# Performance work log

Hardware: AMD Instinct MI355X
Metric: run time of the kernel (lower is better)

## Reference

```python
import jax, jax.numpy as jnp
import numpy as np

WAY, NQ, C, FS = 5, 4096, 64, 5
T = FS * FS            # 25 spatial tokens
EMB = T + 1            # feature_size**2 + feature_proj_dim = 26
HEADS = 2
HD = EMB // HEADS      # 13
SCALE = HD ** -0.5
T_ATTN = 5.0           # args.temperature_attn
TEMP = 0.2             # args.temperature
LN_EPS = 1e-6


def _ln(x, g, b):
    m = x.mean(-1, keepdims=True)
    v = jnp.mean((x - m) ** 2, axis=-1, keepdims=True)
    return (x - m) / jnp.sqrt(v + LN_EPS) * g + b


def _block(x, p):
    # pre-LN transformer block (timm-style), x: (B, T, EMB)
    h = _ln(x, p['ln1_g'], p['ln1_b'])
    qkv = h @ p['qkv_w'].T + p['qkv_b']                       # (B,T,3*EMB)
    B, N, _ = qkv.shape
    qkv = qkv.reshape(B, N, 3, HEADS, HD).transpose(2, 0, 3, 1, 4)
    q, k, v = qkv[0], qkv[1], qkv[2]                          # (B,H,T,hd)
    a = jax.nn.softmax(jnp.einsum('bhqd,bhkd->bhqk', q, k) * SCALE, axis=-1)
    o = jnp.einsum('bhqk,bhkd->bhqd', a, v).transpose(0, 2, 1, 3).reshape(B, N, EMB)
    x = x + o @ p['attn_w'].T + p['attn_b']
    h = _ln(x, p['ln2_g'], p['ln2_b'])
    h = jax.nn.gelu(h @ p['fc1_w'].T + p['fc1_b'], approximate=False)
    return x + h @ p['fc2_w'].T + p['fc2_b']


def _decoder(corr, src, tgt, p):
    # CATs TransformerAggregator, num_hyperpixel=1, depth=1
    # corr: (B,1,T,T); src/tgt: (B,1,T,1) projected features
    pos = jnp.concatenate([
        jnp.broadcast_to(p['pos_x'], (1, 1, FS, FS, EMB // 2)),
        jnp.broadcast_to(p['pos_y'], (1, 1, FS, FS, EMB // 2))], axis=-1).reshape(1, 1, T, EMB)
    B = corr.shape[0]
    x = jnp.concatenate([jnp.swapaxes(corr, -1, -2), tgt], axis=3) + pos
    x = _block(x.reshape(B, T, EMB), p)
    x = (x @ p['dec_w'].T + p['dec_b']).reshape(B, 1, T, T)
    x = jnp.swapaxes(x, -1, -2) + corr            # swap axes for second self-attn pass
    x = jnp.concatenate([x, src], axis=3) + pos
    x = _block(x.reshape(B, T, EMB), p)           # same block weights reused
    x = (x @ p['dec_w'].T + p['dec_b']).reshape(B, 1, T, T) + corr
    return x.mean(axis=1)                         # (B,T,T)


def _forward(spt, qry, proj_w, proj_b, pos_x, pos_y, ln1_g, ln1_b, qkv_w, qkv_b,
             attn_w, attn_b, ln2_g, ln2_b, fc1_w, fc1_b, fc2_w, fc2_b, dec_w, dec_b):
    p = dict(pos_x=pos_x, pos_y=pos_y, ln1_g=ln1_g, ln1_b=ln1_b, qkv_w=qkv_w,
             qkv_b=qkv_b, attn_w=attn_w, attn_b=attn_b, ln2_g=ln2_g, ln2_b=ln2_b,
             fc1_w=fc1_w, fc1_b=fc1_b, fc2_w=fc2_w, fc2_b=fc2_b, dec_w=dec_w, dec_b=dec_b)
    # normalize_feature: subtract channel mean
    spt = spt - spt.mean(axis=1, keepdims=True)
    qry = qry - qry.mean(axis=1, keepdims=True)
    spt_f = jnp.broadcast_to(spt[None], (NQ, WAY, C, FS, FS)).reshape(-1, C, FS, FS)
    qry_f = jnp.broadcast_to(qry[:, None], (NQ, WAY, C, FS, FS)).reshape(-1, C, FS, FS)

    def l2n(x):  # FeatureL2Norm over channel dim
        return x / jnp.sqrt(jnp.sum(x * x, axis=1, keepdims=True) + 1e-6)

    s = l2n(spt_f).reshape(-1, C, T)
    t = l2n(qry_f).reshape(-1, C, T)
    corr = jnp.einsum('bci,bcj->bij', s, t)[:, None]                  # (B,1,T,T)
    sp = (jnp.swapaxes(spt_f.reshape(-1, C, T), 1, 2) @ proj_w.T + proj_b)[:, None]
    tp = (jnp.swapaxes(qry_f.reshape(-1, C, T), 1, 2) @ proj_w.T + proj_b)[:, None]
    refined = _decoder(corr, sp, tp, p)                               # (B,T,T)

    corr_s = refined.reshape(NQ, WAY, T, FS, FS)
    corr_q = refined.reshape(NQ, WAY, FS, FS, T)

    def gnorm(x, axis):  # torch.var is unbiased (ddof=1)
        m = x.mean(axis=axis, keepdims=True)
        v = jnp.var(x, axis=axis, keepdims=True, ddof=1)
        return (x - m) / jnp.sqrt(v + 1e-5)

    corr_s = jax.nn.softmax(gnorm(corr_s, 2) / T_ATTN, axis=2).reshape(NQ, WAY, FS, FS, FS, FS)
    corr_q = jax.nn.softmax(gnorm(corr_q, 4) / T_ATTN, axis=4).reshape(NQ, WAY, FS, FS, FS, FS)
    attn_s = corr_s.sum(axis=(4, 5))                                  # (NQ,WAY,FS,FS)
    attn_q = corr_q.sum(axis=(2, 3))
    spt_att = attn_s[:, :, None] * spt[None]                          # (NQ,WAY,C,FS,FS)
    qry_att = attn_q[:, :, None] * qry[:, None]
    sp_p = spt_att.mean(axis=(-1, -2))                                # (NQ,WAY,C)
    qp_p = qry_att.mean(axis=(-1, -2))
    n1 = jnp.maximum(jnp.linalg.norm(sp_p, axis=-1), 1e-8)
    n2 = jnp.maximum(jnp.linalg.norm(qp_p, axis=-1), 1e-8)
    sim = jnp.sum(sp_p * qp_p, axis=-1) / (n1 * n2)                   # (NQ,WAY)
    return sim / TEMP


def setup_inputs() -> dict:
    key = jax.random.key(0)
    ks = jax.random.split(key, 12)

    def w(i, shape, s=0.02):
        return jax.random.normal(ks[i], shape, jnp.float32) * s

    return {
        'spt': jax.random.normal(ks[0], (WAY, C, FS, FS), jnp.float32),
        'qry': jax.random.normal(ks[1], (NQ, C, FS, FS), jnp.float32),
        'proj_w': w(2, (1, C)), 'proj_b': jnp.zeros((1,), jnp.float32),
        'pos_x': w(3, (1, 1, 1, FS, EMB // 2)),
        'pos_y': w(4, (1, 1, FS, 1, EMB // 2)),
        'ln1_g': jnp.ones((EMB,), jnp.float32), 'ln1_b': jnp.zeros((EMB,), jnp.float32),
        'qkv_w': w(5, (3 * EMB, EMB)), 'qkv_b': jnp.zeros((3 * EMB,), jnp.float32),
        'attn_w': w(6, (EMB, EMB)), 'attn_b': jnp.zeros((EMB,), jnp.float32),
        'ln2_g': jnp.ones((EMB,), jnp.float32), 'ln2_b': jnp.zeros((EMB,), jnp.float32),
        'fc1_w': w(7, (4 * EMB, EMB)), 'fc1_b': jnp.zeros((4 * EMB,), jnp.float32),
        'fc2_w': w(8, (EMB, 4 * EMB)), 'fc2_b': jnp.zeros((EMB,), jnp.float32),
        'dec_w': w(9, (T, EMB)), 'dec_b': jnp.zeros((T,), jnp.float32),
    }


def reference(spt, qry, proj_w, proj_b, pos_x, pos_y, ln1_g, ln1_b, qkv_w, qkv_b,
              attn_w, attn_b, ln2_g, ln2_b, fc1_w, fc1_b, fc2_w, fc2_b, dec_w, dec_b):
    return _forward(spt, qry, proj_w, proj_b, pos_x, pos_y, ln1_g, ln1_b, qkv_w, qkv_b,
                    attn_w, attn_b, ln2_g, ln2_b, fc1_w, fc1_b, fc2_w, fc2_b, dec_w, dec_b)
```

## Files before the change

### kernel.cpp

```cpp
#include <hip/hip_runtime.h>
#include <math.h>

#define WAYS 5
#define NQN 4096
#define NBATCH (NQN*WAYS)
#define SAB 68

#define WS_SC 0
#define WS_RS 8000
#define WS_SP 8125
#define WS_QM 8250
#define WS_QR 110650
#define WS_TP 213050

#define P_L1G 0
#define P_L1B 26
#define P_L2G 52
#define P_L2B 78
#define P_QKVB 104
#define P_ATTB 182
#define P_FC1B 208
#define P_FC2B 312
#define P_DECB 338
#define P_TOT 363

__global__ void prep_spt(const float* __restrict__ spt, const float* __restrict__ proj_w,
                         const float* __restrict__ proj_b, float* __restrict__ ws) {
    int tid = threadIdx.x;
    if (tid >= 125) return;
    int w = tid / 25, i = tid % 25;
    const float* base = spt + w * 1600 + i;
    float s = 0.f;
    for (int c = 0; c < 64; c++) s += base[c * 25];
    float m = s * (1.f / 64.f);
    float ss = 0.f, pj = 0.f;
    for (int c = 0; c < 64; c++) {
        float v = base[c * 25] - m;
        ss += v * v; pj += v * proj_w[c];
        ws[WS_SC + (w * 25 + i) * 64 + c] = v;
    }
    ws[WS_RS + w * 25 + i] = rsqrtf(ss + 1e-6f);
    ws[WS_SP + w * 25 + i] = pj + proj_b[0];
}

__global__ void prep_qry(const float* __restrict__ qry, const float* __restrict__ proj_w,
                         const float* __restrict__ proj_b, float* __restrict__ ws) {
    int idx = blockIdx.x * 256 + threadIdx.x;
    if (idx >= NQN * 25) return;
    int q = idx / 25, j = idx % 25;
    const float* base = qry + q * 1600 + j;
    float s = 0.f;
    for (int c = 0; c < 64; c++) s += base[c * 25];
    float m = s * (1.f / 64.f);
    float ss = 0.f, pj = 0.f;
    for (int c = 0; c < 64; c++) {
        float v = base[c * 25] - m;
        ss += v * v; pj += v * proj_w[c];
    }
    ws[WS_QM + idx] = m;
    ws[WS_QR + idx] = rsqrtf(ss + 1e-6f);
    ws[WS_TP + idx] = pj + proj_b[0];
}

template<int M, int N, int K, int TM, int TN, int SA, int WN, int WK, int SO, int VW,
         bool ADD, bool GELU>
__device__ __forceinline__ void mm(const float* __restrict__ A, const float* __restrict__ W,
                                   const float* __restrict__ bias, float* __restrict__ O,
                                   float scale, int tid) {
    static_assert(M % TM == 0 && N % TN == 0, "tile");
    static_assert(VW == 1 || (WK == 1 && K % VW == 0 && SA % VW == 0 && WN % VW == 0), "vec");
    constexpr int GM = M / TM, GN = N / TN;
    for (int v = tid; v < GM * GN; v += 256) {
        const int m0 = (v / GN) * TM, n0 = (v % GN) * TN;
        float acc[TM][TN];
#pragma unroll
        for (int a = 0; a < TM; a++)
#pragma unroll
            for (int c = 0; c < TN; c++) acc[a][c] = 0.f;

        if constexpr (VW == 4) {
#pragma unroll
            for (int k = 0; k < K; k += 4) {
                float4 av[TM], wv[TN];
#pragma unroll
                for (int a = 0; a < TM; a++) av[a] = *(const float4*)(A + (m0 + a) * SA + k);
#pragma unroll
                for (int c = 0; c < TN; c++) wv[c] = *(const float4*)(W + (n0 + c) * WN + k);
#pragma unroll
                for (int a = 0; a < TM; a++)
#pragma unroll
                    for (int c = 0; c < TN; c++) {
                        acc[a][c] += av[a].x * wv[c].x;
                        acc[a][c] += av[a].y * wv[c].y;
                        acc[a][c] += av[a].z * wv[c].z;
                        acc[a][c] += av[a].w * wv[c].w;
                    }
            }
        } else if constexpr (VW == 2) {
#pragma unroll 4
            for (int k = 0; k < K; k += 2) {
                float2 av[TM], wv[TN];
#pragma unroll
                for (int a = 0; a < TM; a++) av[a] = *(const float2*)(A + (m0 + a) * SA + k);
#pragma unroll
                for (int c = 0; c < TN; c++) wv[c] = *(const float2*)(W + (n0 + c) * WN + k);
#pragma unroll
                for (int a = 0; a < TM; a++)
#pragma unroll
                    for (int c = 0; c < TN; c++) {
                        acc[a][c] += av[a].x * wv[c].x;
                        acc[a][c] += av[a].y * wv[c].y;
                    }
            }
        } else {
#pragma unroll 4
            for (int k = 0; k < K; k++) {
                float av[TM], wv[TN];
#pragma unroll
                for (int a = 0; a < TM; a++) av[a] = A[(m0 + a) * SA + k];
#pragma unroll
                for (int c = 0; c < TN; c++) wv[c] = W[(n0 + c) * WN + k * WK];
#pragma unroll
                for (int a = 0; a < TM; a++)
#pragma unroll
                    for (int c = 0; c < TN; c++) acc[a][c] += av[a] * wv[c];
            }
        }
#pragma unroll
        for (int a = 0; a < TM; a++)
#pragma unroll
            for (int c = 0; c < TN; c++) {
                int n = n0 + c;
                float r = acc[a][c] * scale + (bias ? bias[n] : 0.f);
                if (GELU) r = 0.5f * r * (1.f + erff(r * 0.70710678118654752f));
                if (ADD) O[(m0 + a) * SO + n] += r; else O[(m0 + a) * SO + n] = r;
            }
    }
}

__device__ __forceinline__ void ln_row(const float* __restrict__ x, float* __restrict__ h,
                                       const float* __restrict__ g, const float* __restrict__ bb) {
    float s = 0.f;
#pragma unroll
    for (int e = 0; e < 26; e++) s += x[e];
    float m = s * (1.f / 26.f);
    float vv = 0.f;
#pragma unroll
    for (int e = 0; e < 26; e++) { float d = x[e] - m; vv += d * d; }
    float r = rsqrtf(vv * (1.f / 26.f) + 1e-6f);
#pragma unroll
    for (int e = 0; e < 26; e++) h[e] = (x[e] - m) * r * g[e] + bb[e];
}

__device__ __forceinline__ void xblock(float* __restrict__ xm, float* __restrict__ hm,
                                       float* __restrict__ scr, float* __restrict__ ym,
                                       const float* __restrict__ cpar,
                                       const float* __restrict__ qkv_w,
                                       const float* __restrict__ attn_w,
                                       const float* __restrict__ fc1_w,
                                       const float* __restrict__ fc2_w, int tid) {
    if (tid < 25) ln_row(xm + tid * 26, hm + tid * 26, cpar + P_L1G, cpar + P_L1B);
    __syncthreads();
    mm<25, 78, 26, 5, 3, 26, 26, 1, 78, 2, false, false>(hm, qkv_w, cpar + P_QKVB, scr, 1.f, tid);
    __syncthreads();
    {
        const float SC = 0.27735009811261457f;
        for (int v = tid; v < 250; v += 256) {
            int h = v / 125, r = v % 125;
            int m0 = (r / 25) * 5, j = r % 25;
            const float* kb = scr + j * 78 + 26 + h * 13;
            float acc[5] = {0.f, 0.f, 0.f, 0.f, 0.f};
#pragma unroll
            for (int k = 0; k < 13; k++) {
                float kv = kb[k];
#pragma unroll
                for (int a = 0; a < 5; a++) acc[a] += scr[(m0 + a) * 78 + h * 13 + k] * kv;
            }
            float* orow = ym + h * 625;
#pragma unroll
            for (int a = 0; a < 5; a++) orow[(m0 + a) * 25 + j] = acc[a] * SC;
        }
    }
    __syncthreads();
    if (tid < 50) {
        float* row = ym + (tid / 25) * 625 + (tid % 25) * 25;
        float mx = row[0];
        for (int j = 1; j < 25; j++) mx = fmaxf(mx, row[j]);
        float s = 0.f;
        for (int j = 0; j < 25; j++) { float e = __expf(row[j] - mx); row[j] = e; s += e; }
        float inv = 1.f / s;
        for (int j = 0; j < 25; j++) row[j] *= inv;
    }
    __syncthreads();
    for (int v = tid; v < 130; v += 256) {
        int h = v / 65, r = v % 65;
        int m0 = (r / 13) * 5, n = r % 13;
        const float* P = ym + h * 625;
        float acc[5] = {0.f, 0.f, 0.f, 0.f, 0.f};
#pragma unroll
        for (int k = 0; k < 25; k++) {
            float vv = scr[k * 78 + 52 + h * 13 + n];
#pragma unroll
            for (int a = 0; a < 5; a++) acc[a] += P[(m0 + a) * 25 + k] * vv;
        }
#pragma unroll
        for (int a = 0; a < 5; a++) scr[1950 + (m0 + a) * 26 + h * 13 + n] = acc[a];
    }
    __syncthreads();
    mm<25, 26, 26, 5, 2, 26, 26, 1, 26, 2, true, false>(scr + 1950, attn_w, cpar + P_ATTB, xm, 1.f, tid);
    __syncthreads();
    if (tid < 25) ln_row(xm + tid * 26, hm + tid * 26, cpar + P_L2G, cpar + P_L2B);
    __syncthreads();
    mm<25, 104, 26, 5, 4, 26, 26, 1, 104, 2, false, true>(hm, fc1_w, cpar + P_FC1B, scr, 1.f, tid);
    __syncthreads();
    mm<25, 26, 104, 5, 2, 104, 104, 1, 26, 2, true, false>(scr, fc2_w, cpar + P_FC2B, xm, 1.f, tid);
    __syncthreads();
}

__global__ void __launch_bounds__(256, 4)
fused_kernel(const float* __restrict__ qry, const float* __restrict__ ws,
             const float* __restrict__ pos_x, const float* __restrict__ pos_y,
             const float* __restrict__ qkv_w, const float* __restrict__ qkv_b,
             const float* __restrict__ attn_w, const float* __restrict__ attn_b,
             const float* __restrict__ ln1_g, const float* __restrict__ ln1_b,
             const float* __restrict__ ln2_g, const float* __restrict__ ln2_b,
             const float* __restrict__ fc1_w, const float* __restrict__ fc1_b,
             const float* __restrict__ fc2_w, const float* __restrict__ fc2_b,
             const float* __restrict__ dec_w, const float* __restrict__ dec_b,
             float* __restrict__ out) {
    __shared__ __align__(16) float sc[25 * SAB];
    __shared__ __align__(16) float tcb[25 * SAB];
    __shared__ float rsv[25], rtv[25], spv[25], tpv[25];
    __shared__ __align__(16) float corrm[625];
    __shared__ __align__(16) float xm[650];
    __shared__ __align__(16) float hm[650];
    __shared__ __align__(16) float scr[2600];
    __shared__ __align__(16) float ym[1250];
    __shared__ float asv[25], aqv[25];
    __shared__ __align__(16) float cpar[P_TOT];

    const int b = blockIdx.x, q = b / WAYS, w = b % WAYS, tid = threadIdx.x;

    if (tid < 26) {
        cpar[P_L1G + tid] = ln1_g[tid]; cpar[P_L1B + tid] = ln1_b[tid];
        cpar[P_L2G + tid] = ln2_g[tid]; cpar[P_L2B + tid] = ln2_b[tid];
        cpar[P_ATTB + tid] = attn_b[tid]; cpar[P_FC2B + tid] = fc2_b[tid];
    }
    if (tid < 78) cpar[P_QKVB + tid] = qkv_b[tid];
    if (tid < 104) cpar[P_FC1B + tid] = fc1_b[tid];
    if (tid < 25) cpar[P_DECB + tid] = dec_b[tid];

    for (int e = tid; e < 1600; e += 256) {
        int i = e >> 6, c = e & 63;
        sc[i * SAB + c] = ws[WS_SC + w * 1600 + e] * ws[WS_RS + w * 25 + i];
    }
    if (tid < 25) {
        rsv[tid] = ws[WS_RS + w * 25 + tid];
        spv[tid] = ws[WS_SP + w * 25 + tid];
        rtv[tid] = ws[WS_QR + q * 25 + tid];
        tpv[tid] = ws[WS_TP + q * 25 + tid];
    }
    for (int e = tid; e < 1600; e += 256) {
        int c = e / 25, j = e % 25;
        tcb[j * SAB + c] = (qry[q * 1600 + e] - ws[WS_QM + q * 25 + j]) * ws[WS_QR + q * 25 + j];
    }
    __syncthreads();

    mm<25, 25, 64, 5, 1, SAB, SAB, 1, 25, 4, false, false>(sc, tcb, nullptr, corrm, 1.f, tid);
    __syncthreads();

    for (int e = tid; e < 650; e += 256) {
        int t = e / 26, d = e % 26;
        float p = (d < 13) ? pos_x[(t % 5) * 13 + d] : pos_y[(t / 5) * 13 + (d - 13)];
        float base = (d < 25) ? corrm[d * 25 + t] : tpv[t];
        xm[e] = base + p;
    }
    __syncthreads();

    xblock(xm, hm, scr, ym, cpar, qkv_w, attn_w, fc1_w, fc2_w, tid);

    mm<25, 25, 26, 5, 1, 26, 26, 1, 25, 2, false, false>(xm, dec_w, cpar + P_DECB, ym, 1.f, tid);
    __syncthreads();

    for (int e = tid; e < 650; e += 256) {
        int t = e / 26, d = e % 26;
        float p = (d < 13) ? pos_x[(t % 5) * 13 + d] : pos_y[(t / 5) * 13 + (d - 13)];
        float base = (d < 25) ? (ym[d * 25 + t] + corrm[t * 25 + d]) : spv[t];
        xm[e] = base + p;
    }
    __syncthreads();

    xblock(xm, hm, scr, ym, cpar, qkv_w, attn_w, fc1_w, fc2_w, tid);

    mm<25, 25, 26, 5, 1, 26, 26, 1, 25, 2, false, false>(xm, dec_w, cpar + P_DECB, ym, 1.f, tid);
    __syncthreads();
    for (int e = tid; e < 625; e += 256) ym[e] += corrm[e];
    __syncthreads();

    if (tid < 25) {
        int j = tid;
        float s = 0.f;
        for (int i = 0; i < 25; i++) s += ym[i * 25 + j];
        float m = s * 0.04f;
        float ss = 0.f;
        for (int i = 0; i < 25; i++) { float d = ym[i * 25 + j] - m; ss += d * d; }
        float rinv = rsqrtf(ss * (1.f / 24.f) + 1e-5f) * 0.2f;
        float mx = -1e30f;
        for (int i = 0; i < 25; i++) { float z = (ym[i * 25 + j] - m) * rinv; corrm[i * 25 + j] = z; mx = fmaxf(mx, z); }
        float se = 0.f;
        for (int i = 0; i < 25; i++) { float e2 = __expf(corrm[i * 25 + j] - mx); corrm[i * 25 + j] = e2; se += e2; }
        float inv = 1.f / se;
        for (int i = 0; i < 25; i++) corrm[i * 25 + j] *= inv;
    }
    __syncthreads();
    if (tid < 25) {
        int i = tid; float s = 0.f;
        for (int j = 0; j < 25; j++) s += corrm[i * 25 + j];
        asv[i] = s * 0.04f / rsv[i];
    }
    __syncthreads();
    if (tid < 25) {
        int i = tid;
        float s = 0.f;
        for (int j = 0; j < 25; j++) s += ym[i * 25 + j];
        float m = s * 0.04f;
        float ss = 0.f;
        for (int j = 0; j < 25; j++) { float d = ym[i * 25 + j] - m; ss += d * d; }
        float rinv = rsqrtf(ss * (1.f / 24.f) + 1e-5f) * 0.2f;
        float mx = -1e30f;
        for (int j = 0; j < 25; j++) { float z = (ym[i * 25 + j] - m) * rinv; corrm[i * 25 + j] = z; mx = fmaxf(mx, z); }
        float se = 0.f;
        for (int j = 0; j < 25; j++) { float e2 = __expf(corrm[i * 25 + j] - mx); corrm[i * 25 + j] = e2; se += e2; }
        float inv = 1.f / se;
        for (int j = 0; j < 25; j++) corrm[i * 25 + j] *= inv;
    }
    __syncthreads();
    if (tid < 25) {
        int j = tid; float s = 0.f;
        for (int i = 0; i < 25; i++) s += corrm[i * 25 + j];
        aqv[j] = s * 0.04f / rtv[j];
    }
    __syncthreads();

    if (tid < 64) {
        float s = 0.f;
        for (int i = 0; i < 25; i++) s += asv[i] * sc[i * SAB + tid];
        ym[tid] = s;
        float s2 = 0.f;
        for (int j = 0; j < 25; j++) s2 += aqv[j] * tcb[j * SAB + tid];
        ym[64 + tid] = s2;
    }
    __syncthreads();
    if (tid == 0) {
        float d = 0.f, n1 = 0.f, n2 = 0.f;
        for (int c = 0; c < 64; c++) {
            float a = ym[c], bb2 = ym[64 + c];
            d += a * bb2; n1 += a * a; n2 += bb2 * bb2;
        }
        n1 = fmaxf(sqrtf(n1), 1e-8f);
        n2 = fmaxf(sqrtf(n2), 1e-8f);
        out[b] = d / (n1 * n2) * 5.f;
    }
}

extern "C" void kernel_launch(void* const* d_in, const int* in_sizes, int n_in,
                              void* d_out, int out_size, void* d_ws, size_t ws_size,
                              hipStream_t stream) {
    const float* spt    = (const float*)d_in[0];
    const float* qry    = (const float*)d_in[1];
    const float* proj_w = (const float*)d_in[2];
    const float* proj_b = (const float*)d_in[3];
    const float* pos_x  = (const float*)d_in[4];
    const float* pos_y  = (const float*)d_in[5];
    const float* ln1_g  = (const float*)d_in[6];
    const float* ln1_b  = (const float*)d_in[7];
    const float* qkv_w  = (const float*)d_in[8];
    const float* qkv_b  = (const float*)d_in[9];
    const float* attn_w = (const float*)d_in[10];
    const float* attn_b = (const float*)d_in[11];
    const float* ln2_g  = (const float*)d_in[12];
    const float* ln2_b  = (const float*)d_in[13];
    const float* fc1_w  = (const float*)d_in[14];
    const float* fc1_b  = (const float*)d_in[15];
    const float* fc2_w  = (const float*)d_in[16];
    const float* fc2_b  = (const float*)d_in[17];
    const float* dec_w  = (const float*)d_in[18];
    const float* dec_b  = (const float*)d_in[19];
    float* ws  = (float*)d_ws;
    float* out = (float*)d_out;

    prep_spt<<<1, 128, 0, stream>>>(spt, proj_w, proj_b, ws);
    prep_qry<<<(NQN * 25 + 255) / 256, 256, 0, stream>>>(qry, proj_w, proj_b, ws);
    fused_kernel<<<NBATCH, 256, 0, stream>>>(qry, ws, pos_x, pos_y, qkv_w, qkv_b, attn_w, attn_b,
                                             ln1_g, ln1_b, ln2_g, ln2_b, fc1_w, fc1_b,
                                             fc2_w, fc2_b, dec_w, dec_b, out);
}
```

Before: 1.279 ms.

## Shrink shared memory footprint to raise occupancy and split MLP into halves

Removes the staged parameter cache and the hm buffer and reuses ym and scr regions for the LN output and the attention output. The MLP hidden layer is split into two 52-wide chunks so the scratch buffer can shrink, and launch bounds are raised to 5 blocks per CU. The final cosine reduction now uses a wavefront shuffle instead of a serial single-thread loop. The MLP split adds an extra barrier pair per block, and bias and LN parameters are now read from global memory rather than LDS.

```diff
diff --git a/kernel.cpp b/kernel.cpp
--- a/kernel.cpp
+++ b/kernel.cpp
@@ -12,17 +12,6 @@
 #define WS_QM 8250
 #define WS_QR 110650
 #define WS_TP 213050
-
-#define P_L1G 0
-#define P_L1B 26
-#define P_L2G 52
-#define P_L2B 78
-#define P_QKVB 104
-#define P_ATTB 182
-#define P_FC1B 208
-#define P_FC2B 312
-#define P_DECB 338
-#define P_TOT 363
 
 __global__ void prep_spt(const float* __restrict__ spt, const float* __restrict__ proj_w,
                          const float* __restrict__ proj_b, float* __restrict__ ws) {
@@ -152,16 +141,17 @@
     for (int e = 0; e < 26; e++) h[e] = (x[e] - m) * r * g[e] + bb[e];
 }
 
-__device__ __forceinline__ void xblock(float* __restrict__ xm, float* __restrict__ hm,
-                                       float* __restrict__ scr, float* __restrict__ ym,
-                                       const float* __restrict__ cpar,
-                                       const float* __restrict__ qkv_w,
-                                       const float* __restrict__ attn_w,
-                                       const float* __restrict__ fc1_w,
-                                       const float* __restrict__ fc2_w, int tid) {
-    if (tid < 25) ln_row(xm + tid * 26, hm + tid * 26, cpar + P_L1G, cpar + P_L1B);
-    __syncthreads();
-    mm<25, 78, 26, 5, 3, 26, 26, 1, 78, 2, false, false>(hm, qkv_w, cpar + P_QKVB, scr, 1.f, tid);
+__device__ __forceinline__ void xblock(
+        float* __restrict__ xm, float* __restrict__ scr, float* __restrict__ ym,
+        const float* __restrict__ qkv_w, const float* __restrict__ qkv_b,
+        const float* __restrict__ attn_w, const float* __restrict__ attn_b,
+        const float* __restrict__ ln1_g, const float* __restrict__ ln1_b,
+        const float* __restrict__ ln2_g, const float* __restrict__ ln2_b,
+        const float* __restrict__ fc1_w, const float* __restrict__ fc1_b,
+        const float* __restrict__ fc2_w, const float* __restrict__ fc2_b, int tid) {
+    if (tid < 25) ln_row(xm + tid * 26, ym + tid * 26, ln1_g, ln1_b);
+    __syncthreads();
+    mm<25, 78, 26, 5, 3, 26, 26, 1, 78, 2, false, false>(ym, qkv_w, qkv_b, scr, 1.f, tid);
     __syncthreads();
     {
         const float SC = 0.27735009811261457f;
@@ -204,20 +194,24 @@
             for (int a = 0; a < 5; a++) acc[a] += P[(m0 + a) * 25 + k] * vv;
         }
 #pragma unroll
-        for (int a = 0; a < 5; a++) scr[1950 + (m0 + a) * 26 + h * 13 + n] = acc[a];
-    }
-    __syncthreads();
-    mm<25, 26, 26, 5, 2, 26, 26, 1, 26, 2, true, false>(scr + 1950, attn_w, cpar + P_ATTB, xm, 1.f, tid);
-    __syncthreads();
-    if (tid < 25) ln_row(xm + tid * 26, hm + tid * 26, cpar + P_L2G, cpar + P_L2B);
-    __syncthreads();
-    mm<25, 104, 26, 5, 4, 26, 26, 1, 104, 2, false, true>(hm, fc1_w, cpar + P_FC1B, scr, 1.f, tid);
-    __syncthreads();
-    mm<25, 26, 104, 5, 2, 104, 104, 1, 26, 2, true, false>(scr, fc2_w, cpar + P_FC2B, xm, 1.f, tid);
-    __syncthreads();
-}
-
-__global__ void __launch_bounds__(256, 4)
+        for (int a = 0; a < 5; a++) scr[(m0 + a) * 78 + h * 13 + n] = acc[a];
+    }
+    __syncthreads();
+    mm<25, 26, 26, 5, 2, 78, 26, 1, 26, 2, true, false>(scr, attn_w, attn_b, xm, 1.f, tid);
+    __syncthreads();
+    if (tid < 25) ln_row(xm + tid * 26, ym + tid * 26, ln2_g, ln2_b);
+    __syncthreads();
+    for (int hh = 0; hh < 2; hh++) {
+        mm<25, 52, 26, 5, 4, 26, 26, 1, 78, 2, false, true>(
+            ym, fc1_w + hh * 52 * 26, fc1_b + hh * 52, scr + 26, 1.f, tid);
+        __syncthreads();
+        mm<25, 26, 52, 5, 2, 78, 104, 1, 26, 2, true, false>(
+            scr + 26, fc2_w + hh * 52, hh == 0 ? fc2_b : nullptr, xm, 1.f, tid);
+        __syncthreads();
+    }
+}
+
+__global__ void __launch_bounds__(256, 5)
 fused_kernel(const float* __restrict__ qry, const float* __restrict__ ws,
              const float* __restrict__ pos_x, const float* __restrict__ pos_y,
              const float* __restrict__ qkv_w, const float* __restrict__ qkv_b,
@@ -230,29 +224,17 @@
              float* __restrict__ out) {
     __shared__ __align__(16) float sc[25 * SAB];
     __shared__ __align__(16) float tcb[25 * SAB];
-    __shared__ float rsv[25], rtv[25], spv[25], tpv[25];
-    __shared__ __align__(16) float corrm[625];
-    __shared__ __align__(16) float xm[650];
-    __shared__ __align__(16) float hm[650];
-    __shared__ __align__(16) float scr[2600];
-    __shared__ __align__(16) float ym[1250];
-    __shared__ float asv[25], aqv[25];
-    __shared__ __align__(16) float cpar[P_TOT];
+    __shared__ __align__(16) float corrm[628];
+    __shared__ __align__(16) float xm[652];
+    __shared__ __align__(16) float scr[1952];
+    __shared__ __align__(16) float ym[1252];
+    __shared__ float rsv[25], rtv[25], spv[25], tpv[25], asv[25], aqv[25];
 
     const int b = blockIdx.x, q = b / WAYS, w = b % WAYS, tid = threadIdx.x;
-
-    if (tid < 26) {
-        cpar[P_L1G + tid] = ln1_g[tid]; cpar[P_L1B + tid] = ln1_b[tid];
-        cpar[P_L2G + tid] = ln2_g[tid]; cpar[P_L2B + tid] = ln2_b[tid];
-        cpar[P_ATTB + tid] = attn_b[tid]; cpar[P_FC2B + tid] = fc2_b[tid];
-    }
-    if (tid < 78) cpar[P_QKVB + tid] = qkv_b[tid];
-    if (tid < 104) cpar[P_FC1B + tid] = fc1_b[tid];
-    if (tid < 25) cpar[P_DECB + tid] = dec_b[tid];
 
     for (int e = tid; e < 1600; e += 256) {
         int i = e >> 6, c = e & 63;
-        sc[i * SAB + c] = ws[WS_SC + w * 1600 + e] * ws[WS_RS + w * 25 + i];
+        sc[i * SAB + c] = ws[WS_SC + w * 1600 + e] * ws[WS_RS + w * 25 + (e >> 6)];
     }
     if (tid < 25) {
         rsv[tid] = ws[WS_RS + w * 25 + tid];
@@ -277,9 +259,10 @@
     }
     __syncthreads();
 
-    xblock(xm, hm, scr, ym, cpar, qkv_w, attn_w, fc1_w, fc2_w, tid);
-
-    mm<25, 25, 26, 5, 1, 26, 26, 1, 25, 2, false, false>(xm, dec_w, cpar + P_DECB, ym, 1.f, tid);
+    xblock(xm, scr, ym, qkv_w, qkv_b, attn_w, attn_b, ln1_g, ln1_b, ln2_g, ln2_b,
+           fc1_w, fc1_b, fc2_w, fc2_b, tid);
+
+    mm<25, 25, 26, 5, 1, 26, 26, 1, 25, 2, false, false>(xm, dec_w, dec_b, ym, 1.f, tid);
     __syncthreads();
 
     for (int e = tid; e < 650; e += 256) {
@@ -290,9 +273,10 @@
     }
     __syncthreads();
 
-    xblock(xm, hm, scr, ym, cpar, qkv_w, attn_w, fc1_w, fc2_w, tid);
-
-    mm<25, 25, 26, 5, 1, 26, 26, 1, 25, 2, false, false>(xm, dec_w, cpar + P_DECB, ym, 1.f, tid);
+    xblock(xm, scr, ym, qkv_w, qkv_b, attn_w, attn_b, ln1_g, ln1_b, ln2_g, ln2_b,
+           fc1_w, fc1_b, fc2_w, fc2_b, tid);
+
+    mm<25, 25, 26, 5, 1, 26, 26, 1, 25, 2, false, false>(xm, dec_w, dec_b, ym, 1.f, tid);
     __syncthreads();
     for (int e = tid; e < 625; e += 256) ym[e] += corrm[e];
     __syncthreads();
@@ -343,23 +327,21 @@
     __syncthreads();
 
     if (tid < 64) {
-        float s = 0.f;
-        for (int i = 0; i < 25; i++) s += asv[i] * sc[i * SAB + tid];
-        ym[tid] = s;
-        float s2 = 0.f;
-        for (int j = 0; j < 25; j++) s2 += aqv[j] * tcb[j * SAB + tid];
-        ym[64 + tid] = s2;
-    }
-    __syncthreads();
-    if (tid == 0) {
-        float d = 0.f, n1 = 0.f, n2 = 0.f;
-        for (int c = 0; c < 64; c++) {
-            float a = ym[c], bb2 = ym[64 + c];
-            d += a * bb2; n1 += a * a; n2 += bb2 * bb2;
-        }
-        n1 = fmaxf(sqrtf(n1), 1e-8f);
-        n2 = fmaxf(sqrtf(n2), 1e-8f);
-        out[b] = d / (n1 * n2) * 5.f;
+        int c = tid;
+        float sp = 0.f, qp = 0.f;
+        for (int i = 0; i < 25; i++) sp += asv[i] * sc[i * SAB + c];
+        for (int j = 0; j < 25; j++) qp += aqv[j] * tcb[j * SAB + c];
+        float dp = sp * qp, a2 = sp * sp, b2 = qp * qp;
+        for (int off = 32; off > 0; off >>= 1) {
+            dp += __shfl_xor(dp, off);
+            a2 += __shfl_xor(a2, off);
+            b2 += __shfl_xor(b2, off);
+        }
+        if (tid == 0) {
+            float n1 = fmaxf(sqrtf(a2), 1e-8f);
+            float n2 = fmaxf(sqrtf(b2), 1e-8f);
+            out[b] = dp / (n1 * n2) * 5.f;
+        }
     }
 }
 
```

Result: slower. 1.610 ms (+25.9%).
